# Performance work log

Hardware: AMD Instinct MI355X
Metric: run time of the kernel (lower is better)

Reference implementation:

```python
import jax, jax.numpy as jnp
import numpy as np

D, A, V, H, FFH = 512, 256, 256, 1, 256
B, S, VOCAB = 4096, 50, 100000


def _layer_norm(x, g, b, eps=1e-6):
    mu = jnp.mean(x, axis=-1, keepdims=True)
    var = jnp.mean((x - mu) ** 2, axis=-1, keepdims=True)
    return (x - mu) / jnp.sqrt(var + eps) * g + b


def setup_inputs() -> dict:
    key = jax.random.key(0)
    ks = jax.random.split(key, 12)
    s = 0.02
    return {
        "embed_table": jax.random.normal(ks[0], (VOCAB, D), jnp.float32),
        "idx": jax.random.randint(ks[1], (B, S), 0, VOCAB, dtype=jnp.int32),
        "lengths": jax.random.randint(ks[2], (B,), 0, S, dtype=jnp.int32),
        "W1": jax.random.normal(ks[3], (D, FFH), jnp.float32) * s,
        "b1": jnp.zeros((FFH,), jnp.float32),
        "W2": jax.random.normal(ks[4], (FFH, D), jnp.float32) * s,
        "b2": jnp.zeros((D,), jnp.float32),
        "ln1_g": jnp.ones((D,), jnp.float32),
        "ln1_b": jnp.zeros((D,), jnp.float32),
        "W_qkv": jax.random.normal(ks[5], (D, 2 * A + V), jnp.float32) * s,
        "b_qkv": jnp.zeros((2 * A + V,), jnp.float32),
        "W_o": jax.random.normal(ks[6], (V, D), jnp.float32) * s,
        "b_o": jnp.zeros((D,), jnp.float32),
        "ln2_g": jnp.ones((D,), jnp.float32),
        "ln2_b": jnp.zeros((D,), jnp.float32),
    }


def reference(embed_table, idx, lengths, W1, b1, W2, b2, ln1_g, ln1_b,
              W_qkv, b_qkv, W_o, b_o, ln2_g, ln2_b):
    # neighbor validity mask; guaranteed >= 1 valid neighbor per node
    mask = jnp.arange(S)[None, :] <= lengths[:, None]          # [B,S] bool

    # irregular gather of neighbor embeddings into padded tensor
    x = embed_table[idx]                                       # [B,S,D]

    # FeedForward (relu -> linear) + residual + LayerNorm
    ff = jnp.maximum(jnp.einsum('bsd,df->bsf', x, W1) + b1, 0.0)
    ff = jnp.einsum('bsf,fd->bsd', ff, W2) + b2
    ff = _layer_norm(ff + x, ln1_g, ln1_b)                     # [B,S,D]

    # MultiHeadSelfAttention (combined QKV projection)
    qkv = jnp.einsum('bsd,dc->bsc', ff, W_qkv) + b_qkv         # [B,S,2A+V]
    q, k, v = qkv[..., :A], qkv[..., A:2 * A], qkv[..., 2 * A:]
    q = q.reshape(B, S, H, A // H)
    k = k.reshape(B, S, H, A // H)
    v = v.reshape(B, S, H, V // H)
    scale = jnp.asarray(np.sqrt(D // H), q.dtype)              # AllenNLP scale
    scores = jnp.einsum('bqhd,bkhd->bhqk', q / scale, k)       # [B,H,S,S]
    scores = jnp.where(mask[:, None, None, :], scores, jnp.asarray(-1e9, scores.dtype))
    attn = jax.nn.softmax(scores, axis=-1)
    ctx = jnp.einsum('bhqk,bkhd->bqhd', attn, v).reshape(B, S, V)
    attn_out = jnp.einsum('bsv,vd->bsd', ctx, W_o) + b_o

    out = _layer_norm(attn_out + ff, ln2_g, ln2_b)             # [B,S,D]

    # masked mean pool over neighbors
    m = mask[..., None].astype(out.dtype)                      # [B,S,1]
    pooled = jnp.sum(out * m, axis=1) / jnp.maximum(jnp.sum(m, axis=1), 1e-13)
    return pooled                                              # [B,D]
```

## Files before the change

kernel.cpp:

```cpp
#include <hip/hip_runtime.h>

typedef __bf16 bf16x8 __attribute__((ext_vector_type(8)));
typedef float float4v __attribute__((ext_vector_type(4)));
typedef unsigned short ushort4v __attribute__((ext_vector_type(4)));
typedef unsigned short ushort8v __attribute__((ext_vector_type(8)));

#define K_D 512
#define K_S 50

__device__ __forceinline__ float b2f(unsigned short u) {
  union { unsigned int u32; float f; } v; v.u32 = ((unsigned int)u) << 16; return v.f;
}
__device__ __forceinline__ unsigned short f2b(float f) {
  __bf16 h = (__bf16)f;
  return __builtin_bit_cast(unsigned short, h);
}

__device__ __forceinline__ bf16x8 ldfrag(const unsigned short* buf, int E, int r0, int k0, int lane) {
  int row = r0 + (lane & 15);
  int kb = (k0 + ((lane >> 4) << 3)) << 1;
  return *(const bf16x8*)(buf + row * E + ((kb ^ ((row & 7) << 4)) >> 1));
}

__global__ void prep_weights(const float* __restrict__ src, unsigned short* __restrict__ dst,
                             int K, int N) {
  int KT = K >> 5;
  int total = (N >> 4) * KT * 64;
  int t = blockIdx.x * blockDim.x + threadIdx.x;
  if (t >= total) return;
  int l = t & 63;
  int kt = (t >> 6) % KT;
  int nt = (t >> 6) / KT;
  int kbase = kt * 32 + ((l >> 4) << 3);
  int col = nt * 16 + (l & 15);
  ushort8v o;
  #pragma unroll
  for (int j = 0; j < 8; ++j) o[j] = f2b(src[(size_t)(kbase + j) * N + col]);
  *(ushort8v*)(dst + (size_t)t * 8) = o;
}

template<int NT, int KS, int MT, int SLOTS>
__device__ __forceinline__ void mmN(const unsigned short* Ab, int EA,
                                    const bf16x8* __restrict__ Wf, int wnb, int KT, int l,
                                    float4v* acc) {
  if constexpr (SLOTS == 2) {
    bf16x8 p0[NT], p1[NT];
    #pragma unroll
    for (int n = 0; n < NT; ++n) {
      p0[n] = Wf[(size_t)((wnb + n) * KT) * 64 + l];
      p1[n] = Wf[(size_t)((wnb + n) * KT + 1) * 64 + l];
    }
    #pragma unroll 1
    for (int kt = 0; kt < KS; kt += 2) {
      {
        bf16x8 a[MT];
        #pragma unroll
        for (int m = 0; m < MT; ++m) a[m] = ldfrag(Ab, EA, m * 16, kt * 32, l);
        #pragma unroll
        for (int n = 0; n < NT; ++n) {
          #pragma unroll
          for (int m = 0; m < MT; ++m)
            acc[m * NT + n] = __builtin_amdgcn_mfma_f32_16x16x32_bf16(a[m], p0[n], acc[m * NT + n], 0, 0, 0);
        }
        if (kt + 2 < KS) {
          #pragma unroll
          for (int n = 0; n < NT; ++n)
            p0[n] = Wf[(size_t)((wnb + n) * KT + kt + 2) * 64 + l];
        }
      }
      {
        bf16x8 a[MT];
        #pragma unroll
        for (int m = 0; m < MT; ++m) a[m] = ldfrag(Ab, EA, m * 16, (kt + 1) * 32, l);
        #pragma unroll
        for (int n = 0; n < NT; ++n) {
          #pragma unroll
          for (int m = 0; m < MT; ++m)
            acc[m * NT + n] = __builtin_amdgcn_mfma_f32_16x16x32_bf16(a[m], p1[n], acc[m * NT + n], 0, 0, 0);
        }
        if (kt + 3 < KS) {
          #pragma unroll
          for (int n = 0; n < NT; ++n)
            p1[n] = Wf[(size_t)((wnb + n) * KT + kt + 3) * 64 + l];
        }
      }
    }
  } else {
    bf16x8 bn[NT];
    #pragma unroll
    for (int n = 0; n < NT; ++n) bn[n] = Wf[(size_t)((wnb + n) * KT) * 64 + l];
    #pragma unroll 1
    for (int kt = 0; kt < KS; ++kt) {
      bf16x8 a[MT];
      #pragma unroll
      for (int m = 0; m < MT; ++m) a[m] = ldfrag(Ab, EA, m * 16, kt * 32, l);
      #pragma unroll
      for (int n = 0; n < NT; ++n) {
        #pragma unroll
        for (int m = 0; m < MT; ++m)
          acc[m * NT + n] = __builtin_amdgcn_mfma_f32_16x16x32_bf16(a[m], bn[n], acc[m * NT + n], 0, 0, 0);
      }
      if (kt + 1 < KS) {
        #pragma unroll
        for (int n = 0; n < NT; ++n)
          bn[n] = Wf[(size_t)((wnb + n) * KT + kt + 1) * 64 + l];
      }
    }
  }
}

__device__ __forceinline__ void ln_pass(unsigned short* sXbuf, const float* __restrict__ g,
                                        const float* __restrict__ bb, int w, int l) {
  float gv[8], bv[8];
  {
    const float4* g4 = (const float4*)(g + l * 8);
    const float4* b4 = (const float4*)(bb + l * 8);
    float4 a0 = g4[0], a1 = g4[1], c0 = b4[0], c1 = b4[1];
    gv[0] = a0.x; gv[1] = a0.y; gv[2] = a0.z; gv[3] = a0.w;
    gv[4] = a1.x; gv[5] = a1.y; gv[6] = a1.z; gv[7] = a1.w;
    bv[0] = c0.x; bv[1] = c0.y; bv[2] = c0.z; bv[3] = c0.w;
    bv[4] = c1.x; bv[5] = c1.y; bv[6] = c1.z; bv[7] = c1.w;
  }
  #pragma unroll 1
  for (int rr = 0; rr < 4; ++rr) {
    int r = (w << 2) + rr;
    int e = r * 512 + (((l << 4) ^ ((r & 7) << 4)) >> 1);
    ushort8v x = *(const ushort8v*)(sXbuf + e);
    float v[8];
    float s = 0.f, s2 = 0.f;
    #pragma unroll
    for (int j = 0; j < 8; ++j) { v[j] = b2f(x[j]); s += v[j]; s2 += v[j] * v[j]; }
    #pragma unroll
    for (int off = 1; off < 64; off <<= 1) { s += __shfl_xor(s, off); s2 += __shfl_xor(s2, off); }
    float mu = s * (1.f / 512.f);
    float var = s2 * (1.f / 512.f) - mu * mu;
    float rstd = rsqrtf(var + 1e-6f);
    ushort8v o;
    #pragma unroll
    for (int j = 0; j < 8; ++j) o[j] = f2b((v[j] - mu) * rstd * gv[j] + bv[j]);
    *(ushort8v*)(sXbuf + e) = o;
  }
}

template<int MT>
__device__ __forceinline__ void body(
    unsigned short* sX, unsigned short* sQ, unsigned short* sK,
    float* sS, unsigned short* sP,
    const float* __restrict__ embed, const int* __restrict__ gidx,
    const float* __restrict__ b1, const float* __restrict__ b2,
    const float* __restrict__ ln1g, const float* __restrict__ ln1b,
    const float* __restrict__ bqkv, const float* __restrict__ bo,
    const float* __restrict__ ln2g, const float* __restrict__ ln2b,
    const unsigned short* __restrict__ w1f, const unsigned short* __restrict__ w2f,
    const unsigned short* __restrict__ wqkvf, const unsigned short* __restrict__ wof,
    float* __restrict__ out, int tid, int w, int l, int b, int len) {

  constexpr int S2 = (MT <= 3) ? 2 : 1;

  {
    const int sub = tid >> 7;
    const int c0 = (tid & 127) << 2;
    #pragma unroll 2
    for (int it = 0; it < 2 * MT; ++it) {
      int r = it * 8 + sub;
      float4 v = make_float4(0.f, 0.f, 0.f, 0.f);
      if (r <= len) {
        int row = gidx[b * K_S + r];
        v = *(const float4*)(embed + (size_t)row * K_D + c0);
      }
      ushort4v o;
      o[0] = f2b(v.x); o[1] = f2b(v.y); o[2] = f2b(v.z); o[3] = f2b(v.w);
      *(ushort4v*)(sX + r * 512 + (((c0 << 1) ^ ((r & 7) << 4)) >> 1)) = o;
    }
  }
  __syncthreads();

  {
    float4v acc[MT];
    #pragma unroll
    for (int i = 0; i < MT; ++i) acc[i] = (float4v){0.f, 0.f, 0.f, 0.f};
    mmN<1, 16, MT, 2>(sX, 512, (const bf16x8*)w1f, w, 16, l, acc);
    int col = w * 16 + (l & 15);
    float bias = b1[col];
    #pragma unroll
    for (int m = 0; m < MT; ++m) {
      int r0 = m * 16 + ((l >> 4) << 2);
      #pragma unroll
      for (int j = 0; j < 4; ++j) {
        int r = r0 + j;
        float v = fmaxf(acc[m][j] + bias, 0.f);
        sQ[r * 256 + (((col << 1) ^ ((r & 7) << 4)) >> 1)] = f2b(v);
      }
    }
  }
  __syncthreads();

  {
    float4v acc[2 * MT];
    #pragma unroll
    for (int i = 0; i < 2 * MT; ++i) acc[i] = (float4v){0.f, 0.f, 0.f, 0.f};
    mmN<2, 8, MT, S2>(sQ, 256, (const bf16x8*)w2f, w * 2, 8, l, acc);
    #pragma unroll
    for (int n = 0; n < 2; ++n) {
      int col = (w * 2 + n) * 16 + (l & 15);
      float bias = b2[col];
      #pragma unroll
      for (int m = 0; m < MT; ++m) {
        int r0 = m * 16 + ((l >> 4) << 2);
        #pragma unroll
        for (int j = 0; j < 4; ++j) {
          int r = r0 + j;
          int e = r * 512 + (((col << 1) ^ ((r & 7) << 4)) >> 1);
          float v = acc[m * 2 + n][j] + bias + b2f(sX[e]);
          sX[e] = f2b(v);
        }
      }
    }
  }
  __syncthreads();
  if (w < 4 * MT) ln_pass(sX, ln1g, ln1b, w, l);
  __syncthreads();

  {
    const bf16x8* Wf = (const bf16x8*)wqkvf;
    float4v accQ[MT], accK[MT];
    #pragma unroll
    for (int i = 0; i < MT; ++i) {
      accQ[i] = (float4v){0.f, 0.f, 0.f, 0.f};
      accK[i] = (float4v){0.f, 0.f, 0.f, 0.f};
    }
    const size_t baseQ = (size_t)(w) * 16 * 64 + l;
    const size_t baseK = (size_t)(16 + w) * 16 * 64 + l;
    if constexpr (MT <= 2) {
      bf16x8 q0 = Wf[baseQ],       k0 = Wf[baseK];
      bf16x8 q1 = Wf[baseQ + 64],  k1 = Wf[baseK + 64];
      #pragma unroll 1
      for (int kt = 0; kt < 16; kt += 2) {
        {
          bf16x8 a[MT];
          #pragma unroll
          for (int m = 0; m < MT; ++m) a[m] = ldfrag(sX, 512, m * 16, kt * 32, l);
          #pragma unroll
          for (int m = 0; m < MT; ++m) accQ[m] = __builtin_amdgcn_mfma_f32_16x16x32_bf16(a[m], q0, accQ[m], 0, 0, 0);
          #pragma unroll
          for (int m = 0; m < MT; ++m) accK[m] = __builtin_amdgcn_mfma_f32_16x16x32_bf16(a[m], k0, accK[m], 0, 0, 0);
          if (kt + 2 < 16) {
            q0 = Wf[baseQ + (size_t)(kt + 2) * 64];
            k0 = Wf[baseK + (size_t)(kt + 2) * 64];
          }
        }
        {
          bf16x8 a[MT];
          #pragma unroll
          for (int m = 0; m < MT; ++m) a[m] = ldfrag(sX, 512, m * 16, (kt + 1) * 32, l);
          #pragma unroll
          for (int m = 0; m < MT; ++m) accQ[m] = __builtin_amdgcn_mfma_f32_16x16x32_bf16(a[m], q1, accQ[m], 0, 0, 0);
          #pragma unroll
          for (int m = 0; m < MT; ++m) accK[m] = __builtin_amdgcn_mfma_f32_16x16x32_bf16(a[m], k1, accK[m], 0, 0, 0);
          if (kt + 3 < 16) {
            q1 = Wf[baseQ + (size_t)(kt + 3) * 64];
            k1 = Wf[baseK + (size_t)(kt + 3) * 64];
          }
        }
      }
    } else {
      bf16x8 q0 = Wf[baseQ], k0 = Wf[baseK];
      #pragma unroll 1
      for (int kt = 0; kt < 16; ++kt) {
        bf16x8 a[MT];
        #pragma unroll
        for (int m = 0; m < MT; ++m) a[m] = ldfrag(sX, 512, m * 16, kt * 32, l);
        #pragma unroll
        for (int m = 0; m < MT; ++m) accQ[m] = __builtin_amdgcn_mfma_f32_16x16x32_bf16(a[m], q0, accQ[m], 0, 0, 0);
        #pragma unroll
        for (int m = 0; m < MT; ++m) accK[m] = __builtin_amdgcn_mfma_f32_16x16x32_bf16(a[m], k0, accK[m], 0, 0, 0);
        if (kt + 1 < 16) {
          q0 = Wf[baseQ + (size_t)(kt + 1) * 64];
          k0 = Wf[baseK + (size_t)(kt + 1) * 64];
        }
      }
    }
    const float qscale = 0.044194173824159216f;
    int col = w * 16 + (l & 15);
    float biasQ = bqkv[col];
    float biasK = bqkv[256 + col];
    #pragma unroll
    for (int m = 0; m < MT; ++m) {
      int r0 = m * 16 + ((l >> 4) << 2);
      #pragma unroll
      for (int j = 0; j < 4; ++j) {
        int r = r0 + j;
        sQ[r * 256 + (((col << 1) ^ ((r & 7) << 4)) >> 1)] = f2b((accQ[m][j] + biasQ) * qscale);
        sK[r * 256 + (((col << 1) ^ ((r & 7) << 4)) >> 1)] = f2b(accK[m][j] + biasK);
      }
    }
  }
  __syncthreads();

  if ((w >> 2) < MT) {
    float4v acc = (float4v){0.f, 0.f, 0.f, 0.f};
    int n0 = (w & 3) * 16;
    int m0 = (w >> 2) * 16;
    #pragma unroll
    for (int kt = 0; kt < 8; ++kt) {
      bf16x8 bfr = ldfrag(sK, 256, n0, kt * 32, l);
      bf16x8 a = ldfrag(sQ, 256, m0, kt * 32, l);
      acc = __builtin_amdgcn_mfma_f32_16x16x32_bf16(a, bfr, acc, 0, 0, 0);
    }
    int col = n0 + (l & 15);
    int r0 = m0 + ((l >> 4) << 2);
    #pragma unroll
    for (int j = 0; j < 4; ++j) {
      int r = r0 + j;
      sS[r * 64 + (((col << 2) ^ ((r & 7) << 4)) >> 2)] = acc[j];
    }
  }
  float4v accV[MT];
  {
    #pragma unroll
    for (int i = 0; i < MT; ++i) accV[i] = (float4v){0.f, 0.f, 0.f, 0.f};
    mmN<1, 16, MT, 2>(sX, 512, (const bf16x8*)wqkvf, 32 + w, 16, l, accV);
  }
  __syncthreads();

  {
    if (w < 4 * MT) {
      const bool valid = (l <= len);
      #pragma unroll 1
      for (int rr = 0; rr < 4; ++rr) {
        int r = (w << 2) + rr;
        float s = valid ? sS[r * 64 + (((l << 2) ^ ((r & 7) << 4)) >> 2)] : -1e30f;
        float mx = s;
        #pragma unroll
        for (int off = 1; off < 64; off <<= 1) mx = fmaxf(mx, __shfl_xor(mx, off));
        float p = valid ? __expf(s - mx) : 0.f;
        float sum = p;
        #pragma unroll
        for (int off = 1; off < 64; off <<= 1) sum += __shfl_xor(sum, off);
        sP[r * 64 + (((l << 1) ^ ((r & 7) << 4)) >> 1)] = f2b(p / sum);
      }
    }
    int c = w * 16 + (l & 15);
    float biasV = bqkv[512 + c];
    #pragma unroll
    for (int m = 0; m < MT; ++m) {
      int r0 = m * 16 + ((l >> 4) << 2);
      ushort4v o;
      #pragma unroll
      for (int j = 0; j < 4; ++j) o[j] = f2b(accV[m][j] + biasV);
      *(ushort4v*)(sK + c * 64 + (((r0 << 1) ^ ((c & 7) << 4)) >> 1)) = o;
    }
    #pragma unroll
    for (int m = MT; m < 4; ++m) {
      int r0 = m * 16 + ((l >> 4) << 2);
      ushort4v o; o[0] = 0; o[1] = 0; o[2] = 0; o[3] = 0;
      *(ushort4v*)(sK + c * 64 + (((r0 << 1) ^ ((c & 7) << 4)) >> 1)) = o;
    }
  }
  __syncthreads();

  {
    float4v acc[MT];
    #pragma unroll
    for (int i = 0; i < MT; ++i) acc[i] = (float4v){0.f, 0.f, 0.f, 0.f};
    #pragma unroll
    for (int kt = 0; kt < 2; ++kt) {
      bf16x8 bfr = ldfrag(sK, 64, w * 16, kt * 32, l);
      #pragma unroll
      for (int m = 0; m < MT; ++m) {
        bf16x8 a = ldfrag(sP, 64, m * 16, kt * 32, l);
        acc[m] = __builtin_amdgcn_mfma_f32_16x16x32_bf16(a, bfr, acc[m], 0, 0, 0);
      }
    }
    int col = w * 16 + (l & 15);
    #pragma unroll
    for (int m = 0; m < MT; ++m) {
      int r0 = m * 16 + ((l >> 4) << 2);
      #pragma unroll
      for (int j = 0; j < 4; ++j) {
        int r = r0 + j;
        sQ[r * 256 + (((col << 1) ^ ((r & 7) << 4)) >> 1)] = f2b(acc[m][j]);
      }
    }
  }
  __syncthreads();

  {
    float4v acc[2 * MT];
    #pragma unroll
    for (int i = 0; i < 2 * MT; ++i) acc[i] = (float4v){0.f, 0.f, 0.f, 0.f};
    mmN<2, 8, MT, S2>(sQ, 256, (const bf16x8*)wof, w * 2, 8, l, acc);
    #pragma unroll
    for (int n = 0; n < 2; ++n) {
      int col = (w * 2 + n) * 16 + (l & 15);
      float bias = bo[col];
      #pragma unroll
      for (int m = 0; m < MT; ++m) {
        int r0 = m * 16 + ((l >> 4) << 2);
        #pragma unroll
        for (int j = 0; j < 4; ++j) {
          int r = r0 + j;
          int e = r * 512 + (((col << 1) ^ ((r & 7) << 4)) >> 1);
          float v = acc[m * 2 + n][j] + bias + b2f(sX[e]);
          sX[e] = f2b(v);
        }
      }
    }
  }
  __syncthreads();
  if (w < 4 * MT) ln_pass(sX, ln2g, ln2b, w, l);
  __syncthreads();

  {
    int col = tid & 511;
    int half = tid >> 9;
    float sum = 0.f;
    for (int s = half; s <= len; s += 2)
      sum += b2f(sX[s * 512 + (((col << 1) ^ ((s & 7) << 4)) >> 1)]);
    if (half) sS[col] = sum;
    __syncthreads();
    if (!half) out[(size_t)b * K_D + col] = (sum + sS[col]) / (float)(len + 1);
  }
}

__global__ __launch_bounds__(1024, 4)
void fused_block(
    const float* __restrict__ embed, const int* __restrict__ gidx,
    const int* __restrict__ lengths,
    const float* __restrict__ b1, const float* __restrict__ b2,
    const float* __restrict__ ln1g, const float* __restrict__ ln1b,
    const float* __restrict__ bqkv, const float* __restrict__ bo,
    const float* __restrict__ ln2g, const float* __restrict__ ln2b,
    const unsigned short* __restrict__ w1f, const unsigned short* __restrict__ w2f,
    const unsigned short* __restrict__ wqkvf, const unsigned short* __restrict__ wof,
    float* __restrict__ out) {
  __shared__ unsigned short sX[64 * 512];
  __shared__ unsigned short sQ[64 * 256];
  __shared__ unsigned short sK[64 * 256];
  __shared__ float sS[64 * 64];
  __shared__ unsigned short sP[64 * 64];

  const int tid = (int)threadIdx.x;
  const int w = tid >> 6;
  const int l = tid & 63;
  const int b = (int)blockIdx.x;
  const int len = lengths[b];
  const int mt = (len + 16) >> 4;

  switch (mt) {
    case 1: body<1>(sX, sQ, sK, sS, sP, embed, gidx, b1, b2, ln1g, ln1b, bqkv, bo,
                    ln2g, ln2b, w1f, w2f, wqkvf, wof, out, tid, w, l, b, len); break;
    case 2: body<2>(sX, sQ, sK, sS, sP, embed, gidx, b1, b2, ln1g, ln1b, bqkv, bo,
                    ln2g, ln2b, w1f, w2f, wqkvf, wof, out, tid, w, l, b, len); break;
    case 3: body<3>(sX, sQ, sK, sS, sP, embed, gidx, b1, b2, ln1g, ln1b, bqkv, bo,
                    ln2g, ln2b, w1f, w2f, wqkvf, wof, out, tid, w, l, b, len); break;
    default: body<4>(sX, sQ, sK, sS, sP, embed, gidx, b1, b2, ln1g, ln1b, bqkv, bo,
                     ln2g, ln2b, w1f, w2f, wqkvf, wof, out, tid, w, l, b, len); break;
  }
}

extern "C" void kernel_launch(void* const* d_in, const int* in_sizes, int n_in,
                              void* d_out, int out_size, void* d_ws, size_t ws_size,
                              hipStream_t stream) {
  (void)in_sizes; (void)n_in; (void)out_size; (void)ws_size;
  const float* embed = (const float*)d_in[0];
  const int* idx = (const int*)d_in[1];
  const int* lengths = (const int*)d_in[2];
  const float* W1 = (const float*)d_in[3];
  const float* b1 = (const float*)d_in[4];
  const float* W2 = (const float*)d_in[5];
  const float* b2 = (const float*)d_in[6];
  const float* ln1g = (const float*)d_in[7];
  const float* ln1b = (const float*)d_in[8];
  const float* Wqkv = (const float*)d_in[9];
  const float* bqkv = (const float*)d_in[10];
  const float* Wo = (const float*)d_in[11];
  const float* bo = (const float*)d_in[12];
  const float* ln2g = (const float*)d_in[13];
  const float* ln2b = (const float*)d_in[14];

  unsigned short* ws = (unsigned short*)d_ws;
  unsigned short* w1f = ws;
  unsigned short* w2f = ws + 131072;
  unsigned short* wqkvf = ws + 262144;
  unsigned short* wof = ws + 655360;

  prep_weights<<<64, 256, 0, stream>>>(W1, w1f, 512, 256);
  prep_weights<<<64, 256, 0, stream>>>(W2, w2f, 256, 512);
  prep_weights<<<192, 256, 0, stream>>>(Wqkv, wqkvf, 512, 768);
  prep_weights<<<64, 256, 0, stream>>>(Wo, wof, 256, 512);

  fused_block<<<4096, 1024, 0, stream>>>(embed, idx, lengths, b1, b2, ln1g, ln1b,
                                         bqkv, bo, ln2g, ln2b, w1f, w2f, wqkvf, wof,
                                         (float*)d_out);
}
```

Measured before the change: 528.3 us.

## Software-pipeline LDS A-fragment loads and spread LN/softmax rows across all waves

```diff
diff --git a/kernel.cpp b/kernel.cpp
--- a/kernel.cpp
+++ b/kernel.cpp
@@ -39,7 +39,7 @@
   *(ushort8v*)(dst + (size_t)t * 8) = o;
 }
 
-template<int NT, int KS, int MT, int SLOTS>
+template<int NT, int KS, int MT, int SLOTS, int APRE>
 __device__ __forceinline__ void mmN(const unsigned short* Ab, int EA,
                                     const bf16x8* __restrict__ Wf, int wnb, int KT, int l,
                                     float4v* acc) {
@@ -50,38 +50,56 @@
       p0[n] = Wf[(size_t)((wnb + n) * KT) * 64 + l];
       p1[n] = Wf[(size_t)((wnb + n) * KT + 1) * 64 + l];
     }
+    bf16x8 a0[MT], a1[MT];
+    if constexpr (APRE) {
+      #pragma unroll
+      for (int m = 0; m < MT; ++m) {
+        a0[m] = ldfrag(Ab, EA, m * 16, 0, l);
+        a1[m] = ldfrag(Ab, EA, m * 16, 32, l);
+      }
+    }
     #pragma unroll 1
     for (int kt = 0; kt < KS; kt += 2) {
       {
-        bf16x8 a[MT];
-        #pragma unroll
-        for (int m = 0; m < MT; ++m) a[m] = ldfrag(Ab, EA, m * 16, kt * 32, l);
+        if constexpr (!APRE) {
+          #pragma unroll
+          for (int m = 0; m < MT; ++m) a0[m] = ldfrag(Ab, EA, m * 16, kt * 32, l);
+        }
         #pragma unroll
         for (int n = 0; n < NT; ++n) {
           #pragma unroll
           for (int m = 0; m < MT; ++m)
-            acc[m * NT + n] = __builtin_amdgcn_mfma_f32_16x16x32_bf16(a[m], p0[n], acc[m * NT + n], 0, 0, 0);
+            acc[m * NT + n] = __builtin_amdgcn_mfma_f32_16x16x32_bf16(a0[m], p0[n], acc[m * NT + n], 0, 0, 0);
         }
         if (kt + 2 < KS) {
           #pragma unroll
           for (int n = 0; n < NT; ++n)
             p0[n] = Wf[(size_t)((wnb + n) * KT + kt + 2) * 64 + l];
+          if constexpr (APRE) {
+            #pragma unroll
+            for (int m = 0; m < MT; ++m) a0[m] = ldfrag(Ab, EA, m * 16, (kt + 2) * 32, l);
+          }
         }
       }
       {
-        bf16x8 a[MT];
-        #pragma unroll
-        for (int m = 0; m < MT; ++m) a[m] = ldfrag(Ab, EA, m * 16, (kt + 1) * 32, l);
+        if constexpr (!APRE) {
+          #pragma unroll
+          for (int m = 0; m < MT; ++m) a1[m] = ldfrag(Ab, EA, m * 16, (kt + 1) * 32, l);
+        }
         #pragma unroll
         for (int n = 0; n < NT; ++n) {
           #pragma unroll
           for (int m = 0; m < MT; ++m)
-            acc[m * NT + n] = __builtin_amdgcn_mfma_f32_16x16x32_bf16(a[m], p1[n], acc[m * NT + n], 0, 0, 0);
+            acc[m * NT + n] = __builtin_amdgcn_mfma_f32_16x16x32_bf16(a1[m], p1[n], acc[m * NT + n], 0, 0, 0);
         }
         if (kt + 3 < KS) {
           #pragma unroll
           for (int n = 0; n < NT; ++n)
             p1[n] = Wf[(size_t)((wnb + n) * KT + kt + 3) * 64 + l];
+          if constexpr (APRE) {
+            #pragma unroll
+            for (int m = 0; m < MT; ++m) a1[m] = ldfrag(Ab, EA, m * 16, (kt + 3) * 32, l);
+          }
         }
       }
     }
@@ -110,7 +128,7 @@
 }
 
 __device__ __forceinline__ void ln_pass(unsigned short* sXbuf, const float* __restrict__ g,
-                                        const float* __restrict__ bb, int w, int l) {
+                                        const float* __restrict__ bb, int w, int l, int nrows) {
   float gv[8], bv[8];
   {
     const float4* g4 = (const float4*)(g + l * 8);
@@ -122,8 +140,7 @@
     bv[4] = c1.x; bv[5] = c1.y; bv[6] = c1.z; bv[7] = c1.w;
   }
   #pragma unroll 1
-  for (int rr = 0; rr < 4; ++rr) {
-    int r = (w << 2) + rr;
+  for (int r = w; r < nrows; r += 16) {
     int e = r * 512 + (((l << 4) ^ ((r & 7) << 4)) >> 1);
     ushort8v x = *(const ushort8v*)(sXbuf + e);
     float v[8];
@@ -156,6 +173,8 @@
     float* __restrict__ out, int tid, int w, int l, int b, int len) {
 
   constexpr int S2 = (MT <= 3) ? 2 : 1;
+  constexpr int AP1 = (MT <= 3) ? 1 : 0;
+  constexpr int AP2 = (MT <= 2) ? 1 : 0;
 
   {
     const int sub = tid >> 7;
@@ -179,7 +198,7 @@
     float4v acc[MT];
     #pragma unroll
     for (int i = 0; i < MT; ++i) acc[i] = (float4v){0.f, 0.f, 0.f, 0.f};
-    mmN<1, 16, MT, 2>(sX, 512, (const bf16x8*)w1f, w, 16, l, acc);
+    mmN<1, 16, MT, 2, AP1>(sX, 512, (const bf16x8*)w1f, w, 16, l, acc);
     int col = w * 16 + (l & 15);
     float bias = b1[col];
     #pragma unroll
@@ -199,7 +218,7 @@
     float4v acc[2 * MT];
     #pragma unroll
     for (int i = 0; i < 2 * MT; ++i) acc[i] = (float4v){0.f, 0.f, 0.f, 0.f};
-    mmN<2, 8, MT, S2>(sQ, 256, (const bf16x8*)w2f, w * 2, 8, l, acc);
+    mmN<2, 8, MT, S2, AP2>(sQ, 256, (const bf16x8*)w2f, w * 2, 8, l, acc);
     #pragma unroll
     for (int n = 0; n < 2; ++n) {
       int col = (w * 2 + n) * 16 + (l & 15);
@@ -218,7 +237,7 @@
     }
   }
   __syncthreads();
-  if (w < 4 * MT) ln_pass(sX, ln1g, ln1b, w, l);
+  ln_pass(sX, ln1g, ln1b, w, l, 16 * MT);
   __syncthreads();
 
   {
@@ -234,32 +253,36 @@
     if constexpr (MT <= 2) {
       bf16x8 q0 = Wf[baseQ],       k0 = Wf[baseK];
       bf16x8 q1 = Wf[baseQ + 64],  k1 = Wf[baseK + 64];
+      bf16x8 a0[MT], a1[MT];
+      #pragma unroll
+      for (int m = 0; m < MT; ++m) {
+        a0[m] = ldfrag(sX, 512, m * 16, 0, l);
+        a1[m] = ldfrag(sX, 512, m * 16, 32, l);
+      }
       #pragma unroll 1
       for (int kt = 0; kt < 16; kt += 2) {
         {
-          bf16x8 a[MT];
-          #pragma unroll
-          for (int m = 0; m < MT; ++m) a[m] = ldfrag(sX, 512, m * 16, kt * 32, l);
-          #pragma unroll
-          for (int m = 0; m < MT; ++m) accQ[m] = __builtin_amdgcn_mfma_f32_16x16x32_bf16(a[m], q0, accQ[m], 0, 0, 0);
-          #pragma unroll
-          for (int m = 0; m < MT; ++m) accK[m] = __builtin_amdgcn_mfma_f32_16x16x32_bf16(a[m], k0, accK[m], 0, 0, 0);
+          #pragma unroll
+          for (int m = 0; m < MT; ++m) accQ[m] = __builtin_amdgcn_mfma_f32_16x16x32_bf16(a0[m], q0, accQ[m], 0, 0, 0);
+          #pragma unroll
+          for (int m = 0; m < MT; ++m) accK[m] = __builtin_amdgcn_mfma_f32_16x16x32_bf16(a0[m], k0, accK[m], 0, 0, 0);
           if (kt + 2 < 16) {
             q0 = Wf[baseQ + (size_t)(kt + 2) * 64];
             k0 = Wf[baseK + (size_t)(kt + 2) * 64];
+            #pragma unroll
+            for (int m = 0; m < MT; ++m) a0[m] = ldfrag(sX, 512, m * 16, (kt + 2) * 32, l);
           }
         }
         {
-          bf16x8 a[MT];
-          #pragma unroll
-          for (int m = 0; m < MT; ++m) a[m] = ldfrag(sX, 512, m * 16, (kt + 1) * 32, l);
-          #pragma unroll
-          for (int m = 0; m < MT; ++m) accQ[m] = __builtin_amdgcn_mfma_f32_16x16x32_bf16(a[m], q1, accQ[m], 0, 0, 0);
-          #pragma unroll
-          for (int m = 0; m < MT; ++m) accK[m] = __builtin_amdgcn_mfma_f32_16x16x32_bf16(a[m], k1, accK[m], 0, 0, 0);
+          #pragma unroll
+          for (int m = 0; m < MT; ++m) accQ[m] = __builtin_amdgcn_mfma_f32_16x16x32_bf16(a1[m], q1, accQ[m], 0, 0, 0);
+          #pragma unroll
+          for (int m = 0; m < MT; ++m) accK[m] = __builtin_amdgcn_mfma_f32_16x16x32_bf16(a1[m], k1, accK[m], 0, 0, 0);
           if (kt + 3 < 16) {
             q1 = Wf[baseQ + (size_t)(kt + 3) * 64];
             k1 = Wf[baseK + (size_t)(kt + 3) * 64];
+            #pragma unroll
+            for (int m = 0; m < MT; ++m) a1[m] = ldfrag(sX, 512, m * 16, (kt + 3) * 32, l);
           }
         }
       }
@@ -301,11 +324,20 @@
     float4v acc = (float4v){0.f, 0.f, 0.f, 0.f};
     int n0 = (w & 3) * 16;
     int m0 = (w >> 2) * 16;
-    #pragma unroll
-    for (int kt = 0; kt < 8; ++kt) {
-      bf16x8 bfr = ldfrag(sK, 256, n0, kt * 32, l);
-      bf16x8 a = ldfrag(sQ, 256, m0, kt * 32, l);
-      acc = __builtin_amdgcn_mfma_f32_16x16x32_bf16(a, bfr, acc, 0, 0, 0);
+    bf16x8 b0 = ldfrag(sK, 256, n0, 0, l),  aq0 = ldfrag(sQ, 256, m0, 0, l);
+    bf16x8 b1 = ldfrag(sK, 256, n0, 32, l), aq1 = ldfrag(sQ, 256, m0, 32, l);
+    #pragma unroll 1
+    for (int kt = 0; kt < 8; kt += 2) {
+      acc = __builtin_amdgcn_mfma_f32_16x16x32_bf16(aq0, b0, acc, 0, 0, 0);
+      if (kt + 2 < 8) {
+        b0 = ldfrag(sK, 256, n0, (kt + 2) * 32, l);
+        aq0 = ldfrag(sQ, 256, m0, (kt + 2) * 32, l);
+      }
+      acc = __builtin_amdgcn_mfma_f32_16x16x32_bf16(aq1, b1, acc, 0, 0, 0);
+      if (kt + 3 < 8) {
+        b1 = ldfrag(sK, 256, n0, (kt + 3) * 32, l);
+        aq1 = ldfrag(sQ, 256, m0, (kt + 3) * 32, l);
+      }
     }
     int col = n0 + (l & 15);
     int r0 = m0 + ((l >> 4) << 2);
@@ -319,26 +351,23 @@
   {
     #pragma unroll
     for (int i = 0; i < MT; ++i) accV[i] = (float4v){0.f, 0.f, 0.f, 0.f};
-    mmN<1, 16, MT, 2>(sX, 512, (const bf16x8*)wqkvf, 32 + w, 16, l, accV);
-  }
-  __syncthreads();
-
-  {
-    if (w < 4 * MT) {
-      const bool valid = (l <= len);
-      #pragma unroll 1
-      for (int rr = 0; rr < 4; ++rr) {
-        int r = (w << 2) + rr;
-        float s = valid ? sS[r * 64 + (((l << 2) ^ ((r & 7) << 4)) >> 2)] : -1e30f;
-        float mx = s;
-        #pragma unroll
-        for (int off = 1; off < 64; off <<= 1) mx = fmaxf(mx, __shfl_xor(mx, off));
-        float p = valid ? __expf(s - mx) : 0.f;
-        float sum = p;
-        #pragma unroll
-        for (int off = 1; off < 64; off <<= 1) sum += __shfl_xor(sum, off);
-        sP[r * 64 + (((l << 1) ^ ((r & 7) << 4)) >> 1)] = f2b(p / sum);
-      }
+    mmN<1, 16, MT, 2, AP1>(sX, 512, (const bf16x8*)wqkvf, 32 + w, 16, l, accV);
+  }
+  __syncthreads();
+
+  {
+    const bool valid = (l <= len);
+    #pragma unroll 1
+    for (int r = w; r < 16 * MT; r += 16) {
+      float s = valid ? sS[r * 64 + (((l << 2) ^ ((r & 7) << 4)) >> 2)] : -1e30f;
+      float mx = s;
+      #pragma unroll
+      for (int off = 1; off < 64; off <<= 1) mx = fmaxf(mx, __shfl_xor(mx, off));
+      float p = valid ? __expf(s - mx) : 0.f;
+      float sum = p;
+      #pragma unroll
+      for (int off = 1; off < 64; off <<= 1) sum += __shfl_xor(sum, off);
+      sP[r * 64 + (((l << 1) ^ ((r & 7) << 4)) >> 1)] = f2b(p / sum);
     }
     int c = w * 16 + (l & 15);
     float biasV = bqkv[512 + c];
@@ -389,7 +418,7 @@
     float4v acc[2 * MT];
     #pragma unroll
     for (int i = 0; i < 2 * MT; ++i) acc[i] = (float4v){0.f, 0.f, 0.f, 0.f};
-    mmN<2, 8, MT, S2>(sQ, 256, (const bf16x8*)wof, w * 2, 8, l, acc);
+    mmN<2, 8, MT, S2, AP2>(sQ, 256, (const bf16x8*)wof, w * 2, 8, l, acc);
     #pragma unroll
     for (int n = 0; n < 2; ++n) {
       int col = (w * 2 + n) * 16 + (l & 15);
@@ -408,7 +437,7 @@
     }
   }
   __syncthreads();
-  if (w < 4 * MT) ln_pass(sX, ln2g, ln2b, w, l);
+  ln_pass(sX, ln2g, ln2b, w, l, 16 * MT);
   __syncthreads();
 
   {
```

After: 512.0 us. -3.1%, faster.
